# Kernel optimization log

Measured on AMD Instinct MI355X. Metric: run time of the kernel, lower is better.

The kernel has to match this reference:

```python
import jax, jax.numpy as jnp
import numpy as np
from jax import lax

EPS = 1e-5

def _layernorm_c(x, w, b):
    # WithBias LayerNorm over channel dim (to_3d puts C last; equivalent to axis=1 here)
    mu = x.mean(axis=1, keepdims=True)
    var = x.var(axis=1, keepdims=True)
    return (x - mu) / jnp.sqrt(var + EPS) * w[None, :, None, None] + b[None, :, None, None]

def _conv1x1(x, W, b=None):
    y = jnp.einsum('bchw,oc->bohw', x, W)
    if b is not None:
        y = y + b[None, :, None, None]
    return y

def _dwconv3x3(x, k):
    # k: [C, 1, 3, 3], groups = C
    return lax.conv_general_dilated(
        x, k, window_strides=(1, 1), padding='SAME',
        dimension_numbers=('NCHW', 'OIHW', 'NCHW'),
        feature_group_count=k.shape[0])

def setup_inputs() -> dict:
    key = jax.random.key(0)
    B, C, H, W = 4, 128, 96, 256
    ks = jax.random.split(key, 12)
    s = 0.05
    return {
        'x_l': jax.random.normal(ks[0], (B, C, H, W), jnp.float32),
        'x_r': jax.random.normal(ks[1], (B, C, H, W), jnp.float32),
        'Wl_m': jax.random.normal(ks[2], (2 * C, C), jnp.float32) * s,
        'Wr_m': jax.random.normal(ks[3], (2 * C, C), jnp.float32) * s,
        'dw_l': jax.random.normal(ks[4], (2 * C, 1, 3, 3), jnp.float32) * s,
        'dw_r': jax.random.normal(ks[5], (2 * C, 1, 3, 3), jnp.float32) * s,
        'lnl_w': jnp.ones((C,), jnp.float32),
        'lnl_b': jnp.zeros((C,), jnp.float32),
        'lnr_w': jnp.ones((C,), jnp.float32),
        'lnr_b': jnp.zeros((C,), jnp.float32),
        'Wq_l': jax.random.normal(ks[6], (C, C), jnp.float32) * s,
        'bq_l': jnp.zeros((C,), jnp.float32),
        'Wq_r': jax.random.normal(ks[7], (C, C), jnp.float32) * s,
        'bq_r': jnp.zeros((C,), jnp.float32),
        'beta': jax.random.normal(ks[8], (1, C, 1, 1), jnp.float32) * s,
        'gamma': jax.random.normal(ks[9], (1, C, 1, 1), jnp.float32) * s,
    }

def reference(x_l, x_r, Wl_m, Wr_m, dw_l, dw_r, lnl_w, lnl_b, lnr_w, lnr_b,
              Wq_l, bq_l, Wq_r, bq_r, beta, gamma):
    c = x_l.shape[1]
    scale = c ** -0.5
    fusion_l = _dwconv3x3(_conv1x1(x_l, Wl_m), dw_l)   # [b,2c,h,w]
    V_l, l_mid = jnp.split(fusion_l, 2, axis=1)
    fusion_r = _dwconv3x3(_conv1x1(x_r, Wr_m), dw_r)
    V_r, r_mid = jnp.split(fusion_r, 2, axis=1)
    Q_l = _conv1x1(_layernorm_c(l_mid, lnl_w, lnl_b), Wq_l, bq_l)  # [b,c,h,w]
    Q_r = _conv1x1(_layernorm_c(r_mid, lnr_w, lnr_b), Wq_r, bq_r)  # [b,c,h,w]
    # row-wise attention over width: [b,h,w,w]
    attn = jnp.einsum('bchw,bchv->bhwv', Q_l, Q_r) * scale
    # F_r2l: softmax over last axis (v), contract V_r over v
    F_r2l = jnp.einsum('bhwv,bchv->bchw', jax.nn.softmax(attn, axis=-1), V_r)
    # F_l2r: softmax of attn^T over its last axis == softmax over w (axis=-2)
    F_l2r = jnp.einsum('bhwv,bchw->bchv', jax.nn.softmax(attn, axis=-2), V_l)
    out_l = x_l + F_r2l * beta
    out_r = x_r + F_l2r * gamma
    return (out_l, out_r)
```

## Files before the change

### kernel.cpp

```cpp
#include <hip/hip_runtime.h>
#include <hip/hip_bf16.h>

using bf16 = __hip_bfloat16;
typedef __attribute__((ext_vector_type(8))) short bf16x8;
typedef __attribute__((ext_vector_type(2))) float f32x2;
typedef __attribute__((ext_vector_type(4))) float f32x4;
typedef __attribute__((ext_vector_type(16))) float f32x16;
typedef __attribute__((ext_vector_type(4))) unsigned int u32x4;

#define DEVI __device__ __forceinline__

constexpr int B = 4, C = 128, C2 = 256, H = 96, W = 256;
constexpr int HW = H * W;
constexpr int NPIX = B * HW;
constexpr int BH = B * H;
constexpr float SCALE = 0.08838834764831845f;
constexpr float LN_EPS = 1e-5f;

DEVI float lo16(unsigned u) { return __builtin_bit_cast(float, u << 16); }
DEVI float hi16(unsigned u) { return __builtin_bit_cast(float, u & 0xffff0000u); }
DEVI unsigned short f2bu(float v) {
    bf16 b = __float2bfloat16(v);
    return __builtin_bit_cast(unsigned short, b);
}
DEVI unsigned packbf2(float a, float b) {
    return (unsigned)f2bu(a) | ((unsigned)f2bu(b) << 16);
}
DEVI f32x2 up2(unsigned p) { return f32x2{lo16(p), hi16(p)}; }

__global__ __launch_bounds__(256) void wcvt_kernel(
    const float* __restrict__ w0, const float* __restrict__ w1,
    const float* __restrict__ w2, const float* __restrict__ w3,
    unsigned short* __restrict__ o0, unsigned short* __restrict__ o1,
    unsigned short* __restrict__ o2, unsigned short* __restrict__ o3)
{
    const int id = blockIdx.x, t = threadIdx.x;
    const float* src; unsigned short* dst; int base;
    if (id < 8)       { src = w0; dst = o0; base = id * 4096; }
    else if (id < 16) { src = w1; dst = o1; base = (id - 8) * 4096; }
    else if (id < 20) { src = w2; dst = o2; base = (id - 16) * 4096; }
    else              { src = w3; dst = o3; base = (id - 20) * 4096; }
#pragma unroll
    for (int u = 0; u < 4; ++u) {
        int i = base + t * 16 + u * 4;
        float4 v = *reinterpret_cast<const float4*>(&src[i]);
        ushort4 o;
        o.x = f2bu(v.x); o.y = f2bu(v.y); o.z = f2bu(v.z); o.w = f2bu(v.w);
        *reinterpret_cast<ushort4*>(&dst[i]) = o;
    }
}

__global__ __launch_bounds__(256) void transpose_kernel(
    const float* __restrict__ x_l, const float* __restrict__ x_r,
    unsigned short* __restrict__ xT_l, unsigned short* __restrict__ xT_r)
{
    __shared__ unsigned short ts[64][132];
    const int side = blockIdx.x & 1;
    const int u = blockIdx.x >> 1;
    const float* x = side ? x_r : x_l;
    unsigned short* xT = side ? xT_r : xT_l;
    const int t = threadIdx.x;
    const int b = u / (HW / 64);
    const int hw0 = (u % (HW / 64)) * 64;
#pragma unroll
    for (int i = 0; i < 8; ++i) {
        int idx = t + i * 256;
        int c = idx >> 4;
        int px = (idx & 15) * 4;
        float4 v = *reinterpret_cast<const float4*>(&x[((size_t)b * C + c) * HW + hw0 + px]);
        ts[px + 0][c] = f2bu(v.x);
        ts[px + 1][c] = f2bu(v.y);
        ts[px + 2][c] = f2bu(v.z);
        ts[px + 3][c] = f2bu(v.w);
    }
    __syncthreads();
#pragma unroll
    for (int i = 0; i < 8; ++i) {
        int idx = t + i * 256;
        int px = idx >> 5;
        int c4 = (idx & 31) * 4;
        ushort4 v = *reinterpret_cast<const ushort4*>(&ts[px][c4]);
        *reinterpret_cast<ushort4*>(&xT[(size_t)(b * HW + hw0 + px) * C + c4]) = v;
    }
}

__global__ __launch_bounds__(256) void conv1x1_mfma_kernel(
    const unsigned short* __restrict__ xT_l, const unsigned short* __restrict__ xT_r,
    const unsigned short* __restrict__ Wb_l, const unsigned short* __restrict__ Wb_r,
    unsigned short* __restrict__ y_l, unsigned short* __restrict__ y_r)
{
    const int side = blockIdx.x & 1;
    const int u = blockIdx.x >> 1;
    const unsigned short* xT = side ? xT_r : xT_l;
    const unsigned short* Wb = side ? Wb_r : Wb_l;
    unsigned short* y = side ? y_r : y_l;

    const int t = threadIdx.x;
    const int lane = t & 63, wid = t >> 6;
    const int wr = wid >> 1, wc = wid & 1;
    const int l15 = lane & 15, l4 = lane >> 4;
    const int pxb = u % 768;
    const int ocb = u / 768;

    const int px_base = pxb * 128 + wr * 64 + l15;
    const int oc_base = ocb * 128 + wc * 64 + l15;

    f32x4 acc[4][4] = {};
    for (int kk = 0; kk < 4; ++kk) {
        const int k0 = kk * 32 + l4 * 8;
        bf16x8 a[4], bb[4];
#pragma unroll
        for (int mt = 0; mt < 4; ++mt)
            a[mt] = *reinterpret_cast<const bf16x8*>(&xT[(size_t)(px_base + mt * 16) * C + k0]);
#pragma unroll
        for (int nt = 0; nt < 4; ++nt)
            bb[nt] = *reinterpret_cast<const bf16x8*>(&Wb[(size_t)(oc_base + nt * 16) * C + k0]);
#pragma unroll
        for (int mt = 0; mt < 4; ++mt)
#pragma unroll
            for (int nt = 0; nt < 4; ++nt)
                acc[mt][nt] = __builtin_amdgcn_mfma_f32_16x16x32_bf16(a[mt], bb[nt], acc[mt][nt], 0, 0, 0);
    }
#pragma unroll
    for (int mt = 0; mt < 4; ++mt)
#pragma unroll
        for (int nt = 0; nt < 4; ++nt) {
            const int oc = ocb * 128 + wc * 64 + nt * 16 + l15;
#pragma unroll
            for (int r = 0; r < 4; ++r) {
                const int px = pxb * 128 + wr * 64 + mt * 16 + l4 * 4 + r;
                y[(size_t)px * C2 + oc] = f2bu(acc[mt][nt][r]);
            }
        }
}

__global__ __launch_bounds__(256, 3) void dwlnq_kernel(
    const unsigned short* __restrict__ y_l, const unsigned short* __restrict__ y_r,
    const float* __restrict__ dwk_l, const float* __restrict__ dwk_r,
    const float* __restrict__ lnw_l, const float* __restrict__ lnb_l,
    const float* __restrict__ lnw_r, const float* __restrict__ lnb_r,
    const unsigned short* __restrict__ Wq_l, const unsigned short* __restrict__ Wq_r,
    const float* __restrict__ bq_l, const float* __restrict__ bq_r,
    unsigned short* __restrict__ VT_l, unsigned short* __restrict__ VT_r,
    unsigned short* __restrict__ q_l, unsigned short* __restrict__ q_r)
{
    __shared__ unsigned short ts[64][128];
    __shared__ unsigned char msb[64 * 256];
    __shared__ float lnwb[256];

    const int side = blockIdx.x & 1;
    const int u = blockIdx.x >> 1;
    const unsigned short* y = side ? y_r : y_l;
    const float* dwk = side ? dwk_r : dwk_l;
    const float* lnw = side ? lnw_r : lnw_l;
    const float* lnb = side ? lnb_r : lnb_l;
    const unsigned short* Wqb = side ? Wq_r : Wq_l;
    const float* bq = side ? bq_r : bq_l;
    unsigned short* VT = side ? VT_r : VT_l;
    unsigned short* q = side ? q_r : q_l;

    const int t = threadIdx.x;
    const int wt = u & 3;
    const int bh = u >> 2;
    const int h = bh % H;
    const int ch8 = t & 31, wi = t >> 5;
    const int c0 = ch8 * 8;
    const int wbase = wt * 64 + wi * 8;

    lnwb[t] = (t < 128) ? lnw[t] : lnb[t - 128];

    f32x2 acc2[8][4] = {};
#pragma unroll
    for (int dh = 0; dh < 3; ++dh) {
        const int hh = h + dh - 1;
        if ((unsigned)hh >= (unsigned)H) continue;
        f32x2 wt0[4], wt1[4], wt2[4];
#pragma unroll
        for (int k = 0; k < 4; ++k) {
            const float* d0 = dwk + (c0 + 2 * k) * 9 + dh * 3;
            const float* d1 = dwk + (c0 + 2 * k + 1) * 9 + dh * 3;
            wt0[k] = f32x2{d0[0], d1[0]};
            wt1[k] = f32x2{d0[1], d1[1]};
            wt2[k] = f32x2{d0[2], d1[2]};
        }
        const unsigned short* yrow = y + (size_t)(bh + dh - 1) * W * C2 + c0;
        uint4 uu[10];
#pragma unroll
        for (int j = 0; j < 10; ++j) {
            const int ww = wbase - 1 + j;
            uint4 v = {0u, 0u, 0u, 0u};
            if ((unsigned)ww < 256u)
                v = *reinterpret_cast<const uint4*>(&yrow[(size_t)ww * C2]);
            uu[j] = v;
        }
#pragma unroll
        for (int j = 0; j < 10; ++j) {
            const unsigned arr[4] = {uu[j].x, uu[j].y, uu[j].z, uu[j].w};
            f32x2 v[4];
#pragma unroll
            for (int k = 0; k < 4; ++k) v[k] = up2(arr[k]);
            if (j < 8) {
#pragma unroll
                for (int k = 0; k < 4; ++k) acc2[j][k] += v[k] * wt0[k];
            }
            if (j >= 1 && j <= 8) {
#pragma unroll
                for (int k = 0; k < 4; ++k) acc2[j - 1][k] += v[k] * wt1[k];
            }
            if (j >= 2) {
#pragma unroll
                for (int k = 0; k < 4; ++k) acc2[j - 2][k] += v[k] * wt2[k];
            }
        }
    }

#pragma unroll
    for (int i = 0; i < 8; ++i) {
        uint4 o;
        o.x = packbf2(acc2[i][0].x, acc2[i][0].y);
        o.y = packbf2(acc2[i][1].x, acc2[i][1].y);
        o.z = packbf2(acc2[i][2].x, acc2[i][2].y);
        o.w = packbf2(acc2[i][3].x, acc2[i][3].y);
        const int pxl = wi * 8 + i;
        if (c0 < 128) {
            *reinterpret_cast<uint4*>(&ts[pxl][c0]) = o;
        } else {
            const unsigned addr = (unsigned)(pxl * 256 + (c0 - 128) * 2) ^ (unsigned)(i << 4);
            *reinterpret_cast<uint4*>(msb + addr) = o;
        }
    }
    __syncthreads();

#pragma unroll
    for (int it = 0; it < 4; ++it) {
        const int idx = t + it * 256;
        const int c = idx & 127, w8 = idx >> 7;
        unsigned short vals[8];
#pragma unroll
        for (int k = 0; k < 8; ++k) vals[k] = ts[w8 * 8 + k][c];
        unsigned short* dst = &VT[((size_t)bh * C + c) * W + wt * 64 + w8 * 8];
        *reinterpret_cast<ushort4*>(dst)     = *reinterpret_cast<const ushort4*>(&vals[0]);
        *reinterpret_cast<ushort4*>(dst + 4) = *reinterpret_cast<const ushort4*>(&vals[4]);
    }

    {
        const int px = t >> 2, qq = t & 3;
        uint4 raw[4];
#pragma unroll
        for (int v = 0; v < 4; ++v) {
            const unsigned addr =
                (unsigned)(px * 256 + qq * 64 + v * 16) ^ (unsigned)((px & 7) << 4);
            raw[v] = *reinterpret_cast<const uint4*>(msb + addr);
        }
        float s1 = 0.f, s2 = 0.f;
#pragma unroll
        for (int v = 0; v < 4; ++v) {
            const unsigned arr[4] = {raw[v].x, raw[v].y, raw[v].z, raw[v].w};
#pragma unroll
            for (int k = 0; k < 4; ++k) {
                float v0 = lo16(arr[k]), v1 = hi16(arr[k]);
                s1 += v0 + v1; s2 += v0 * v0 + v1 * v1;
            }
        }
        s1 += __shfl_xor(s1, 1); s2 += __shfl_xor(s2, 1);
        s1 += __shfl_xor(s1, 2); s2 += __shfl_xor(s2, 2);
        const float mu = s1 * (1.f / C);
        const float rs = rsqrtf(s2 * (1.f / C) - mu * mu + LN_EPS);
#pragma unroll
        for (int v = 0; v < 4; ++v) {
            const unsigned arr[4] = {raw[v].x, raw[v].y, raw[v].z, raw[v].w};
            float nv[8];
#pragma unroll
            for (int k = 0; k < 4; ++k) {
                int c = qq * 32 + v * 8 + k * 2;
                nv[k * 2]     = (lo16(arr[k]) - mu) * rs * lnwb[c] + lnwb[128 + c];
                nv[k * 2 + 1] = (hi16(arr[k]) - mu) * rs * lnwb[c + 1] + lnwb[128 + c + 1];
            }
            uint4 wv;
            wv.x = packbf2(nv[0], nv[1]); wv.y = packbf2(nv[2], nv[3]);
            wv.z = packbf2(nv[4], nv[5]); wv.w = packbf2(nv[6], nv[7]);
            const unsigned addr =
                (unsigned)(px * 256 + qq * 64 + v * 16) ^ (unsigned)((px & 7) << 4);
            *reinterpret_cast<uint4*>(msb + addr) = wv;
        }
    }
    __syncthreads();

    {
        const int lane = t & 63, wid = t >> 6;
        const int l15 = lane & 15, l4 = lane >> 4;
        f32x4 acc[8] = {};
        for (int kk = 0; kk < 4; ++kk) {
            const int k0 = kk * 32 + l4 * 8;
            const int pxl = wid * 16 + l15;
            const unsigned aaddr =
                (unsigned)(pxl * 256 + k0 * 2) ^ (unsigned)((pxl & 7) << 4);
            bf16x8 a = *reinterpret_cast<const bf16x8*>(msb + aaddr);
#pragma unroll
            for (int nt = 0; nt < 8; ++nt) {
                bf16x8 bv = *reinterpret_cast<const bf16x8*>(
                    &Wqb[(size_t)(nt * 16 + l15) * C + k0]);
                acc[nt] = __builtin_amdgcn_mfma_f32_16x16x32_bf16(a, bv, acc[nt], 0, 0, 0);
            }
        }
        const size_t px0 = (size_t)bh * W + wt * 64;
#pragma unroll
        for (int nt = 0; nt < 8; ++nt) {
            const int oc = nt * 16 + l15;
            const float bias = bq[oc];
#pragma unroll
            for (int r = 0; r < 4; ++r) {
                const int pxr = wid * 16 + l4 * 4 + r;
                q[(px0 + pxr) * C + oc] = f2bu(acc[nt][r] + bias);
            }
        }
    }
}

__global__ __launch_bounds__(256, 2) void fused_attn_kernel(
    const unsigned short* __restrict__ Q_l, const unsigned short* __restrict__ Q_r,
    const unsigned short* __restrict__ VT_l, const unsigned short* __restrict__ VT_r,
    const float* __restrict__ x_l, const float* __restrict__ x_r,
    const float* __restrict__ beta, const float* __restrict__ gamma,
    float* __restrict__ out_l, float* __restrict__ out_r)
{
    __shared__ __align__(16) unsigned char lds[65536];
    const int bid = blockIdx.x;
    const int xcd = bid & 7;
    const int local = bid >> 3;
    const int bh = xcd * 48 + (local >> 2);
    const int sub = local & 3;
    const int side = sub & 1, half = sub >> 1;

    const unsigned short* Q  = side ? Q_r : Q_l;
    const unsigned short* K  = side ? Q_l : Q_r;
    const unsigned short* VT = side ? VT_l : VT_r;
    const float* x    = side ? x_r : x_l;
    const float* coef = side ? gamma : beta;
    float* out        = side ? out_r : out_l;

    const int t = threadIdx.x;
    const int lane = t & 63, wv = t >> 6;
    const int l31 = lane & 31, hi = lane >> 5;
    const int b = bh / H, h = bh % H;
    const int w0 = half * 128 + wv * 32;

    const unsigned short* qrow = Q + ((size_t)bh * W + w0 + l31) * C + hi * 8;
    bf16x8 qfrag[8];
#pragma unroll
    for (int ks = 0; ks < 8; ++ks)
        qfrag[ks] = *reinterpret_cast<const bf16x8*>(qrow + ks * 16);

    const char* kg = (const char*)(K + (size_t)bh * W * C);
    const char* vg = (const char*)(VT + (size_t)bh * C * W);
    const int srow = lane >> 4;
    const int scol = (lane & 15) * 16;

    float sden_loc = 0.f;
    f32x16 oacc[4] = {};

    for (int ci = 0; ci < 2; ++ci) {
#pragma unroll
        for (int i = 0; i < 8; ++i) {
            const int r0 = wv * 32 + i * 4;
            const int row = r0 + srow;
            const char* src = kg + (size_t)(ci * 128 + row) * 256 + (scol ^ ((row & 7) << 4));
            __builtin_amdgcn_global_load_lds(
                (const __attribute__((address_space(1))) void*)src,
                (__attribute__((address_space(3))) void*)(lds + r0 * 256), 16, 0, 0);
        }
#pragma unroll
        for (int i = 0; i < 8; ++i) {
            const int r0 = wv * 32 + i * 4;
            const int row = r0 + srow;
            const char* src = vg + (size_t)row * 512 + ci * 256 + (scol ^ ((row & 7) << 4));
            __builtin_amdgcn_global_load_lds(
                (const __attribute__((address_space(1))) void*)src,
                (__attribute__((address_space(3))) void*)(lds + 32768 + r0 * 256), 16, 0, 0);
        }
        __syncthreads();

        f32x16 sacc[4] = {};
        __builtin_amdgcn_s_setprio(1);
#pragma unroll
        for (int vt = 0; vt < 4; ++vt) {
            const int row = vt * 32 + l31;
            const unsigned rb = row * 256;
            const unsigned sw = (row & 7) << 4;
#pragma unroll
            for (int ks = 0; ks < 8; ++ks) {
                bf16x8 a = *reinterpret_cast<const bf16x8*>(
                    lds + rb + ((ks * 32 + hi * 16) ^ sw));
                sacc[vt] = __builtin_amdgcn_mfma_f32_32x32x16_bf16(a, qfrag[ks], sacc[vt], 0, 0, 0);
            }
        }
        __builtin_amdgcn_s_setprio(0);

#pragma unroll
        for (int vt = 0; vt < 4; ++vt)
#pragma unroll
            for (int r = 0; r < 16; ++r) {
                float e = __expf(sacc[vt][r] * SCALE);
                sacc[vt][r] = e;
                sden_loc += e;
            }

        unsigned pw[8][4];
#pragma unroll
        for (int g = 0; g < 8; ++g) {
            const int vt = g >> 1, bs = (g & 1) * 8;
            unsigned pa = packbf2(sacc[vt][bs + 0], sacc[vt][bs + 1]);
            unsigned pc = packbf2(sacc[vt][bs + 2], sacc[vt][bs + 3]);
            unsigned pb = packbf2(sacc[vt][bs + 4], sacc[vt][bs + 5]);
            unsigned pd = packbf2(sacc[vt][bs + 6], sacc[vt][bs + 7]);
            unsigned sa = __shfl_xor(pa, 32);
            unsigned sb = __shfl_xor(pb, 32);
            unsigned sc = __shfl_xor(pc, 32);
            unsigned sd = __shfl_xor(pd, 32);
            pw[g][0] = hi ? sb : pa;
            pw[g][1] = hi ? sd : pc;
            pw[g][2] = hi ? pb : sa;
            pw[g][3] = hi ? pd : sc;
        }

        __builtin_amdgcn_s_setprio(1);
#pragma unroll
        for (int ct = 0; ct < 4; ++ct) {
            const int row = ct * 32 + l31;
            const unsigned rb = 32768 + row * 256;
            const unsigned sw = (row & 7) << 4;
#pragma unroll
            for (int g = 0; g < 8; ++g) {
                bf16x8 va = *reinterpret_cast<const bf16x8*>(
                    lds + rb + ((g * 32 + hi * 16) ^ sw));
                u32x4 pv = {pw[g][0], pw[g][1], pw[g][2], pw[g][3]};
                oacc[ct] = __builtin_amdgcn_mfma_f32_32x32x16_bf16(
                    va, __builtin_bit_cast(bf16x8, pv), oacc[ct], 0, 0, 0);
            }
        }
        __builtin_amdgcn_s_setprio(0);
        __syncthreads();
    }

    const float sden = sden_loc + __shfl_xor(sden_loc, 32);
    const float inv = 1.f / sden;
    const size_t base0 = (size_t)b * C * HW + (size_t)h * W + w0 + l31;
#pragma unroll
    for (int ct = 0; ct < 4; ++ct)
#pragma unroll
        for (int r = 0; r < 16; ++r) {
            const int c = ct * 32 + (r & 3) + 8 * (r >> 2) + 4 * hi;
            const size_t a = base0 + (size_t)c * HW;
            out[a] = x[a] + oacc[ct][r] * inv * coef[c];
        }
}

extern "C" void kernel_launch(void* const* d_in, const int* in_sizes, int n_in,
                              void* d_out, int out_size, void* d_ws, size_t ws_size,
                              hipStream_t stream) {
    (void)in_sizes; (void)n_in; (void)out_size; (void)ws_size;
    const float* x_l   = (const float*)d_in[0];
    const float* x_r   = (const float*)d_in[1];
    const float* Wl_m  = (const float*)d_in[2];
    const float* Wr_m  = (const float*)d_in[3];
    const float* dw_l  = (const float*)d_in[4];
    const float* dw_r  = (const float*)d_in[5];
    const float* lnl_w = (const float*)d_in[6];
    const float* lnl_b = (const float*)d_in[7];
    const float* lnr_w = (const float*)d_in[8];
    const float* lnr_b = (const float*)d_in[9];
    const float* Wq_l  = (const float*)d_in[10];
    const float* bq_l  = (const float*)d_in[11];
    const float* Wq_r  = (const float*)d_in[12];
    const float* bq_r  = (const float*)d_in[13];
    const float* beta  = (const float*)d_in[14];
    const float* gamma = (const float*)d_in[15];

    char* ws = (char*)d_ws;
    unsigned short* ymid_l   = (unsigned short*)(ws + 0);
    unsigned short* ymid_r   = (unsigned short*)(ws + 50331648);
    unsigned short* VT_l     = (unsigned short*)(ws + 150994944);
    unsigned short* VT_r     = (unsigned short*)(ws + 176160768);
    unsigned short* Q_l      = (unsigned short*)(ws + 201326592);
    unsigned short* Q_r      = (unsigned short*)(ws + 226492416);
    unsigned short* Wlb      = (unsigned short*)(ws + 251658240);
    unsigned short* Wrb      = (unsigned short*)(ws + 251723776);
    unsigned short* Wqlb     = (unsigned short*)(ws + 251789312);
    unsigned short* Wqrb     = (unsigned short*)(ws + 251822080);
    unsigned short* xT_l     = Q_l;
    unsigned short* xT_r     = Q_r;

    float* out_l = (float*)d_out;
    float* out_r = out_l + (size_t)B * C * HW;

    const dim3 blk(256);

    wcvt_kernel<<<24, blk, 0, stream>>>(Wl_m, Wr_m, Wq_l, Wq_r, Wlb, Wrb, Wqlb, Wqrb);

    transpose_kernel<<<3072, blk, 0, stream>>>(x_l, x_r, xT_l, xT_r);
    conv1x1_mfma_kernel<<<3072, blk, 0, stream>>>(xT_l, xT_r, Wlb, Wrb, ymid_l, ymid_r);
    dwlnq_kernel<<<3072, blk, 0, stream>>>(ymid_l, ymid_r, dw_l, dw_r,
                                           lnl_w, lnl_b, lnr_w, lnr_b,
                                           Wqlb, Wqrb, bq_l, bq_r,
                                           VT_l, VT_r, Q_l, Q_r);
    fused_attn_kernel<<<1536, blk, 0, stream>>>(Q_l, Q_r, VT_l, VT_r,
                                                x_l, x_r, beta, gamma, out_l, out_r);
}
```

Measured before the change: 247.5 us.

## Compute LayerNorm in registers and write V transpose directly from dwconv accumulators

The V half of the depthwise-conv output is now packed along width in registers and stored straight to the transposed VT buffer, with no round trip through a shared-memory transpose tile. The LayerNorm statistics for the mid half are computed from fp32 accumulators using cross-lane shuffles, and the normalized values are written once into the swizzled shared buffer. This drops one barrier, the ts and lnwb shared arrays, and a shared-memory reread pass. It also removes the occupancy hint from launch bounds. Statistics are now taken from fp32 values rather than bf16-rounded ones, which slightly changes numerics. Half the threads take each branch, and register pressure may rise.

```diff
diff --git a/kernel.cpp b/kernel.cpp
--- a/kernel.cpp
+++ b/kernel.cpp
@@ -134,7 +134,7 @@
         }
 }
 
-__global__ __launch_bounds__(256, 3) void dwlnq_kernel(
+__global__ __launch_bounds__(256) void dwlnq_kernel(
     const unsigned short* __restrict__ y_l, const unsigned short* __restrict__ y_r,
     const float* __restrict__ dwk_l, const float* __restrict__ dwk_r,
     const float* __restrict__ lnw_l, const float* __restrict__ lnb_l,
@@ -144,9 +144,7 @@
     unsigned short* __restrict__ VT_l, unsigned short* __restrict__ VT_r,
     unsigned short* __restrict__ q_l, unsigned short* __restrict__ q_r)
 {
-    __shared__ unsigned short ts[64][128];
     __shared__ unsigned char msb[64 * 256];
-    __shared__ float lnwb[256];
 
     const int side = blockIdx.x & 1;
     const int u = blockIdx.x >> 1;
@@ -167,8 +165,6 @@
     const int c0 = ch8 * 8;
     const int wbase = wt * 64 + wi * 8;
 
-    lnwb[t] = (t < 128) ? lnw[t] : lnb[t - 128];
-
     f32x2 acc2[8][4] = {};
 #pragma unroll
     for (int dh = 0; dh < 3; ++dh) {
@@ -214,74 +210,64 @@
         }
     }
 
-#pragma unroll
-    for (int i = 0; i < 8; ++i) {
-        uint4 o;
-        o.x = packbf2(acc2[i][0].x, acc2[i][0].y);
-        o.y = packbf2(acc2[i][1].x, acc2[i][1].y);
-        o.z = packbf2(acc2[i][2].x, acc2[i][2].y);
-        o.w = packbf2(acc2[i][3].x, acc2[i][3].y);
-        const int pxl = wi * 8 + i;
-        if (c0 < 128) {
-            *reinterpret_cast<uint4*>(&ts[pxl][c0]) = o;
-        } else {
-            const unsigned addr = (unsigned)(pxl * 256 + (c0 - 128) * 2) ^ (unsigned)(i << 4);
+    if (c0 < 128) {
+#pragma unroll
+        for (int k = 0; k < 8; ++k) {
+            uint4 o;
+            o.x = packbf2(acc2[0][k >> 1][k & 1], acc2[1][k >> 1][k & 1]);
+            o.y = packbf2(acc2[2][k >> 1][k & 1], acc2[3][k >> 1][k & 1]);
+            o.z = packbf2(acc2[4][k >> 1][k & 1], acc2[5][k >> 1][k & 1]);
+            o.w = packbf2(acc2[6][k >> 1][k & 1], acc2[7][k >> 1][k & 1]);
+            *reinterpret_cast<uint4*>(&VT[((size_t)bh * C + c0 + k) * W + wbase]) = o;
+        }
+    } else {
+        float s1[8], s2[8];
+#pragma unroll
+        for (int i = 0; i < 8; ++i) {
+            float a = 0.f, b2 = 0.f;
+#pragma unroll
+            for (int k = 0; k < 4; ++k) {
+                a  += acc2[i][k].x + acc2[i][k].y;
+                b2 += acc2[i][k].x * acc2[i][k].x + acc2[i][k].y * acc2[i][k].y;
+            }
+            s1[i] = a; s2[i] = b2;
+        }
+#pragma unroll
+        for (int off = 1; off <= 8; off <<= 1)
+#pragma unroll
+            for (int i = 0; i < 8; ++i) {
+                s1[i] += __shfl_xor(s1[i], off);
+                s2[i] += __shfl_xor(s2[i], off);
+            }
+        const int cm = c0 - 128;
+        float lw[8], lb[8];
+        {
+            float4 a0 = *reinterpret_cast<const float4*>(&lnw[cm]);
+            float4 a1 = *reinterpret_cast<const float4*>(&lnw[cm + 4]);
+            float4 b0 = *reinterpret_cast<const float4*>(&lnb[cm]);
+            float4 b1 = *reinterpret_cast<const float4*>(&lnb[cm + 4]);
+            lw[0] = a0.x; lw[1] = a0.y; lw[2] = a0.z; lw[3] = a0.w;
+            lw[4] = a1.x; lw[5] = a1.y; lw[6] = a1.z; lw[7] = a1.w;
+            lb[0] = b0.x; lb[1] = b0.y; lb[2] = b0.z; lb[3] = b0.w;
+            lb[4] = b1.x; lb[5] = b1.y; lb[6] = b1.z; lb[7] = b1.w;
+        }
+#pragma unroll
+        for (int i = 0; i < 8; ++i) {
+            const float mu = s1[i] * (1.f / C);
+            const float rs = rsqrtf(s2[i] * (1.f / C) - mu * mu + LN_EPS);
+            float nv[8];
+#pragma unroll
+            for (int k = 0; k < 4; ++k) {
+                nv[k * 2]     = (acc2[i][k].x - mu) * rs * lw[k * 2] + lb[k * 2];
+                nv[k * 2 + 1] = (acc2[i][k].y - mu) * rs * lw[k * 2 + 1] + lb[k * 2 + 1];
+            }
+            uint4 o;
+            o.x = packbf2(nv[0], nv[1]); o.y = packbf2(nv[2], nv[3]);
+            o.z = packbf2(nv[4], nv[5]); o.w = packbf2(nv[6], nv[7]);
+            const int pxl = wi * 8 + i;
+            const unsigned addr =
+                (unsigned)(pxl * 256 + cm * 2) ^ (unsigned)((pxl & 7) << 4);
             *reinterpret_cast<uint4*>(msb + addr) = o;
-        }
-    }
-    __syncthreads();
-
-#pragma unroll
-    for (int it = 0; it < 4; ++it) {
-        const int idx = t + it * 256;
-        const int c = idx & 127, w8 = idx >> 7;
-        unsigned short vals[8];
-#pragma unroll
-        for (int k = 0; k < 8; ++k) vals[k] = ts[w8 * 8 + k][c];
-        unsigned short* dst = &VT[((size_t)bh * C + c) * W + wt * 64 + w8 * 8];
-        *reinterpret_cast<ushort4*>(dst)     = *reinterpret_cast<const ushort4*>(&vals[0]);
-        *reinterpret_cast<ushort4*>(dst + 4) = *reinterpret_cast<const ushort4*>(&vals[4]);
-    }
-
-    {
-        const int px = t >> 2, qq = t & 3;
-        uint4 raw[4];
-#pragma unroll
-        for (int v = 0; v < 4; ++v) {
-            const unsigned addr =
-                (unsigned)(px * 256 + qq * 64 + v * 16) ^ (unsigned)((px & 7) << 4);
-            raw[v] = *reinterpret_cast<const uint4*>(msb + addr);
-        }
-        float s1 = 0.f, s2 = 0.f;
-#pragma unroll
-        for (int v = 0; v < 4; ++v) {
-            const unsigned arr[4] = {raw[v].x, raw[v].y, raw[v].z, raw[v].w};
-#pragma unroll
-            for (int k = 0; k < 4; ++k) {
-                float v0 = lo16(arr[k]), v1 = hi16(arr[k]);
-                s1 += v0 + v1; s2 += v0 * v0 + v1 * v1;
-            }
-        }
-        s1 += __shfl_xor(s1, 1); s2 += __shfl_xor(s2, 1);
-        s1 += __shfl_xor(s1, 2); s2 += __shfl_xor(s2, 2);
-        const float mu = s1 * (1.f / C);
-        const float rs = rsqrtf(s2 * (1.f / C) - mu * mu + LN_EPS);
-#pragma unroll
-        for (int v = 0; v < 4; ++v) {
-            const unsigned arr[4] = {raw[v].x, raw[v].y, raw[v].z, raw[v].w};
-            float nv[8];
-#pragma unroll
-            for (int k = 0; k < 4; ++k) {
-                int c = qq * 32 + v * 8 + k * 2;
-                nv[k * 2]     = (lo16(arr[k]) - mu) * rs * lnwb[c] + lnwb[128 + c];
-                nv[k * 2 + 1] = (hi16(arr[k]) - mu) * rs * lnwb[c + 1] + lnwb[128 + c + 1];
-            }
-            uint4 wv;
-            wv.x = packbf2(nv[0], nv[1]); wv.y = packbf2(nv[2], nv[3]);
-            wv.z = packbf2(nv[4], nv[5]); wv.w = packbf2(nv[6], nv[7]);
-            const unsigned addr =
-                (unsigned)(px * 256 + qq * 64 + v * 16) ^ (unsigned)((px & 7) << 4);
-            *reinterpret_cast<uint4*>(msb + addr) = wv;
         }
     }
     __syncthreads();
```

New measurement: 255.3 us. 1.03x slower.

## Fuse input transpose into 1x1 conv MFMA kernel via shared-memory staging

Applied to the files above, without the earlier changes.

Removes the separate transpose kernel. The conv1x1 kernel now loads x directly, converts it to bf16 and transposes it into shared memory, then feeds the MFMAs from LDS. Each block covers 64 pixels and all 256 output channels, one wave per 64 channels. Swapping the MFMA operands lets each lane write four consecutive output channels as one packed store instead of scalar stores. This cuts one launch and the bf16 xT round trip through global memory, but weights are re-read per block. It also changes the XOR swizzle key in dwlnq's shared-memory write to depend on the pixel row.

```diff
diff --git a/kernel.cpp b/kernel.cpp
--- a/kernel.cpp
+++ b/kernel.cpp
@@ -50,60 +50,37 @@
     }
 }
 
-__global__ __launch_bounds__(256) void transpose_kernel(
+__global__ __launch_bounds__(256) void conv1x1_mfma_kernel(
     const float* __restrict__ x_l, const float* __restrict__ x_r,
-    unsigned short* __restrict__ xT_l, unsigned short* __restrict__ xT_r)
+    const unsigned short* __restrict__ Wb_l, const unsigned short* __restrict__ Wb_r,
+    unsigned short* __restrict__ y_l, unsigned short* __restrict__ y_r)
 {
-    __shared__ unsigned short ts[64][132];
+    __shared__ unsigned short xs[64][132];
     const int side = blockIdx.x & 1;
     const int u = blockIdx.x >> 1;
     const float* x = side ? x_r : x_l;
-    unsigned short* xT = side ? xT_r : xT_l;
+    const unsigned short* Wb = side ? Wb_r : Wb_l;
+    unsigned short* y = side ? y_r : y_l;
+
     const int t = threadIdx.x;
     const int b = u / (HW / 64);
     const int hw0 = (u % (HW / 64)) * 64;
+
 #pragma unroll
     for (int i = 0; i < 8; ++i) {
-        int idx = t + i * 256;
-        int c = idx >> 4;
-        int px = (idx & 15) * 4;
-        float4 v = *reinterpret_cast<const float4*>(&x[((size_t)b * C + c) * HW + hw0 + px]);
-        ts[px + 0][c] = f2bu(v.x);
-        ts[px + 1][c] = f2bu(v.y);
-        ts[px + 2][c] = f2bu(v.z);
-        ts[px + 3][c] = f2bu(v.w);
+        const int idx = t + i * 256;
+        const int px4 = (idx & 15) * 4;
+        const int c = idx >> 4;
+        float4 v = *reinterpret_cast<const float4*>(&x[((size_t)b * C + c) * HW + hw0 + px4]);
+        xs[px4 + 0][c] = f2bu(v.x);
+        xs[px4 + 1][c] = f2bu(v.y);
+        xs[px4 + 2][c] = f2bu(v.z);
+        xs[px4 + 3][c] = f2bu(v.w);
     }
     __syncthreads();
-#pragma unroll
-    for (int i = 0; i < 8; ++i) {
-        int idx = t + i * 256;
-        int px = idx >> 5;
-        int c4 = (idx & 31) * 4;
-        ushort4 v = *reinterpret_cast<const ushort4*>(&ts[px][c4]);
-        *reinterpret_cast<ushort4*>(&xT[(size_t)(b * HW + hw0 + px) * C + c4]) = v;
-    }
-}
-
-__global__ __launch_bounds__(256) void conv1x1_mfma_kernel(
-    const unsigned short* __restrict__ xT_l, const unsigned short* __restrict__ xT_r,
-    const unsigned short* __restrict__ Wb_l, const unsigned short* __restrict__ Wb_r,
-    unsigned short* __restrict__ y_l, unsigned short* __restrict__ y_r)
-{
-    const int side = blockIdx.x & 1;
-    const int u = blockIdx.x >> 1;
-    const unsigned short* xT = side ? xT_r : xT_l;
-    const unsigned short* Wb = side ? Wb_r : Wb_l;
-    unsigned short* y = side ? y_r : y_l;
-
-    const int t = threadIdx.x;
+
     const int lane = t & 63, wid = t >> 6;
-    const int wr = wid >> 1, wc = wid & 1;
     const int l15 = lane & 15, l4 = lane >> 4;
-    const int pxb = u % 768;
-    const int ocb = u / 768;
-
-    const int px_base = pxb * 128 + wr * 64 + l15;
-    const int oc_base = ocb * 128 + wc * 64 + l15;
 
     f32x4 acc[4][4] = {};
     for (int kk = 0; kk < 4; ++kk) {
@@ -111,27 +88,29 @@
         bf16x8 a[4], bb[4];
 #pragma unroll
         for (int mt = 0; mt < 4; ++mt)
-            a[mt] = *reinterpret_cast<const bf16x8*>(&xT[(size_t)(px_base + mt * 16) * C + k0]);
+            a[mt] = *reinterpret_cast<const bf16x8*>(&xs[mt * 16 + l15][k0]);
 #pragma unroll
         for (int nt = 0; nt < 4; ++nt)
-            bb[nt] = *reinterpret_cast<const bf16x8*>(&Wb[(size_t)(oc_base + nt * 16) * C + k0]);
+            bb[nt] = *reinterpret_cast<const bf16x8*>(
+                &Wb[(size_t)(wid * 64 + nt * 16 + l15) * C + k0]);
 #pragma unroll
         for (int mt = 0; mt < 4; ++mt)
 #pragma unroll
             for (int nt = 0; nt < 4; ++nt)
-                acc[mt][nt] = __builtin_amdgcn_mfma_f32_16x16x32_bf16(a[mt], bb[nt], acc[mt][nt], 0, 0, 0);
-    }
-#pragma unroll
-    for (int mt = 0; mt < 4; ++mt)
+                acc[mt][nt] = __builtin_amdgcn_mfma_f32_16x16x32_bf16(bb[nt], a[mt], acc[mt][nt], 0, 0, 0);
+    }
+#pragma unroll
+    for (int mt = 0; mt < 4; ++mt) {
+        const size_t px = (size_t)(b * HW + hw0 + mt * 16 + l15);
 #pragma unroll
         for (int nt = 0; nt < 4; ++nt) {
-            const int oc = ocb * 128 + wc * 64 + nt * 16 + l15;
-#pragma unroll
-            for (int r = 0; r < 4; ++r) {
-                const int px = pxb * 128 + wr * 64 + mt * 16 + l4 * 4 + r;
-                y[(size_t)px * C2 + oc] = f2bu(acc[mt][nt][r]);
-            }
-        }
+            const int oc = wid * 64 + nt * 16 + l4 * 4;
+            uint2 o;
+            o.x = packbf2(acc[mt][nt][0], acc[mt][nt][1]);
+            o.y = packbf2(acc[mt][nt][2], acc[mt][nt][3]);
+            *reinterpret_cast<uint2*>(&y[px * C2 + oc]) = o;
+        }
+    }
 }
 
 __global__ __launch_bounds__(256, 3) void dwlnq_kernel(
@@ -225,7 +204,8 @@
         if (c0 < 128) {
             *reinterpret_cast<uint4*>(&ts[pxl][c0]) = o;
         } else {
-            const unsigned addr = (unsigned)(pxl * 256 + (c0 - 128) * 2) ^ (unsigned)(i << 4);
+            const unsigned addr =
+                (unsigned)(pxl * 256 + (c0 - 128) * 2) ^ (unsigned)((pxl & 7) << 4);
             *reinterpret_cast<uint4*>(msb + addr) = o;
         }
     }
@@ -487,8 +467,6 @@
     unsigned short* Wrb      = (unsigned short*)(ws + 251723776);
     unsigned short* Wqlb     = (unsigned short*)(ws + 251789312);
     unsigned short* Wqrb     = (unsigned short*)(ws + 251822080);
-    unsigned short* xT_l     = Q_l;
-    unsigned short* xT_r     = Q_r;
 
     float* out_l = (float*)d_out;
     float* out_r = out_l + (size_t)B * C * HW;
@@ -497,8 +475,7 @@
 
     wcvt_kernel<<<24, blk, 0, stream>>>(Wl_m, Wr_m, Wq_l, Wq_r, Wlb, Wrb, Wqlb, Wqrb);
 
-    transpose_kernel<<<3072, blk, 0, stream>>>(x_l, x_r, xT_l, xT_r);
-    conv1x1_mfma_kernel<<<3072, blk, 0, stream>>>(xT_l, xT_r, Wlb, Wrb, ymid_l, ymid_r);
+    conv1x1_mfma_kernel<<<3072, blk, 0, stream>>>(x_l, x_r, Wlb, Wrb, ymid_l, ymid_r);
     dwlnq_kernel<<<3072, blk, 0, stream>>>(ymid_l, ymid_r, dw_l, dw_r,
                                            lnl_w, lnl_b, lnr_w, lnr_b,
                                            Wqlb, Wqrb, bq_l, bq_r,
```

After: 229.8 us. -7.1%, faster.
